# Performance work log

Hardware: AMD Instinct MI355X
Metric: run time of the kernel (lower is better)

Reference implementation:

```python
import jax, jax.numpy as jnp
import numpy as np

NH, DH = 16, 64          # n_head, d_head
CH = NH + DH             # 80
RQ, RK, RV = 6, 2, 2
ROPE_BASE = 10000.0


def _rotary(b, cache_len):
    # b: [B, T, R, DH]; rotates the d-factor exactly as the torch Rotary module
    T = b.shape[1]
    inv_freq = (1.0 / ROPE_BASE) ** (jnp.arange(0, DH, 2, dtype=jnp.float32) / DH)
    t = jnp.arange(T, dtype=jnp.float32) + cache_len
    freqs = jnp.outer(t, inv_freq)                      # [T, DH/2]
    cos = freqs[None, :, None, :].astype(b.dtype)
    sin = jnp.sin(freqs)[None, :, None, :].astype(b.dtype)
    cos = jnp.cos(freqs)[None, :, None, :].astype(b.dtype)
    x1, x2 = jnp.split(b, 2, axis=3)
    return jnp.concatenate([x1 * cos + x2 * sin, -x1 * sin + x2 * cos], axis=3)


def setup_inputs() -> dict:
    key = jax.random.key(0)
    k1, k2, k3, k4 = jax.random.split(key, 4)
    B, T, D = 2, 2048, 1024
    x = jax.random.normal(k1, (B, T, D), dtype=jnp.float32)
    # xavier-uniform-like scale for factor projections
    s_q = float(np.sqrt(6.0 / (D + CH)))
    s_o = float(np.sqrt(6.0 / (D + D)))
    W_abq = jax.random.uniform(k2, (RQ * CH, D), minval=-s_q, maxval=s_q, dtype=jnp.float32)
    W_abkv = jax.random.uniform(k3, ((RK + RV) * CH, D), minval=-s_q, maxval=s_q, dtype=jnp.float32)
    W_o = jax.random.uniform(k4, (D, D), minval=-s_o, maxval=s_o, dtype=jnp.float32)
    return {"x": x, "W_abq": W_abq, "W_abkv": W_abkv, "W_o": W_o}


def reference(x, W_abq, W_abkv, W_o):
    B, T, D = x.shape
    # low-rank factor projections
    abq = (x @ W_abq.T).reshape(B, T, RQ, CH)
    a_q, b_q = abq[..., :NH], abq[..., NH:]            # [B,T,RQ,NH], [B,T,RQ,DH]
    abkv = (x @ W_abkv.T).reshape(B, T, RK + RV, CH)
    a_kv = abkv[..., :NH]
    b_kv = _rotary(abkv[..., NH:], cache_len=0)        # RoPE applied to K/V d-factors only
    a_k, b_k = a_kv[:, :, :RK], b_kv[:, :, :RK]
    a_v, b_v = a_kv[:, :, RK:], b_kv[:, :, RK:]
    # tensor-product reconstruction of Q/K/V
    q = jnp.einsum('btrh,btrd->bthd', a_q, b_q) / RQ
    k = jnp.einsum('btrh,btrd->bthd', a_k, b_k) / RK
    v = jnp.einsum('btrh,btrd->bthd', a_v, b_v) / RV
    # causal attention (flex_attention default scale = 1/sqrt(dh))
    scale = 1.0 / jnp.sqrt(jnp.asarray(DH, dtype=q.dtype))
    scores = jnp.einsum('bqhd,bkhd->bhqk', q, k) * scale
    causal = jnp.tril(jnp.ones((T, T), dtype=bool))
    scores = jnp.where(causal[None, None], scores, jnp.finfo(scores.dtype).min)
    attn = jax.nn.softmax(scores, axis=-1)
    y = jnp.einsum('bhqk,bkhd->bqhd', attn, v).reshape(B, T, D)
    return y @ W_o.T
```

## Files before the change

### kernel.cpp

```cpp
#include <hip/hip_runtime.h>
#include <hip/hip_bf16.h>
#include <math.h>

#define NHEADS 16
#define DHEAD  64
#define CHDIM  80
#define RQn    6
#define RKn    2
#define RVn    2
#define BB     2
#define TT     2048
#define DDim   1024
#define NQK    800

using frag16 = __attribute__((ext_vector_type(8))) short;
using f32x4  = __attribute__((ext_vector_type(4))) float;
using f32x16 = __attribute__((ext_vector_type(16))) float;

#define AS1(p) ((const __attribute__((address_space(1))) unsigned int*)(p))
#define AS3(p) ((__attribute__((address_space(3))) unsigned int*)(p))

static __device__ __forceinline__ unsigned short bf16_bits(float f) {
    __hip_bfloat16 h = __float2bfloat16(f);
    return *(unsigned short*)&h;
}
static __device__ __forceinline__ unsigned int pk2(float a, float b) {
    return ((unsigned int)bf16_bits(b) << 16) | (unsigned int)bf16_bits(a);
}

__global__ __launch_bounds__(256) void cvt_all(
    const float* __restrict__ x, const float* __restrict__ wq,
    const float* __restrict__ wk, const float* __restrict__ wo,
    __hip_bfloat16* __restrict__ xb, __hip_bfloat16* __restrict__ wqk,
    __hip_bfloat16* __restrict__ wob)
{
    int bid = blockIdx.x;
    const float* src; __hip_bfloat16* dst; int n4;
    if (bid < 4096)      { src = x;  dst = xb;            n4 = 1048576; }
    else if (bid < 4576) { bid -= 4096; src = wq; dst = wqk;           n4 = 122880; }
    else if (bid < 4896) { bid -= 4576; src = wk; dst = wqk + 491520;  n4 = 81920; }
    else                 { bid -= 4896; src = wo; dst = wob;           n4 = 262144; }
    int i = bid * 256 + threadIdx.x;
    if (i < n4) {
        float4 v = *(const float4*)&src[i * 4];
        ushort4 o;
        o.x = bf16_bits(v.x); o.y = bf16_bits(v.y);
        o.z = bf16_bits(v.z); o.w = bf16_bits(v.w);
        *(ushort4*)&dst[i * 4] = o;
    }
}

__global__ __launch_bounds__(256) void gemm_bf16(
    const __hip_bfloat16* __restrict__ A, const __hip_bfloat16* __restrict__ W,
    float* __restrict__ C, int M, int N, int K)
{
    __shared__ __hip_bfloat16 Asl[2][128 * 64];
    __shared__ __hip_bfloat16 Bsl[2][128 * 64];
    const int tid = threadIdx.x;
    const int w = tid >> 6, lane = tid & 63;
    const int l16 = lane & 15, quad = lane >> 4;
    const int wr = w >> 1, wc = w & 1;
    const int bm = blockIdx.y * 128, bn = blockIdx.x * 128;

    int rS[4], cS[4], rBS[4];
    #pragma unroll
    for (int j = 0; j < 4; j++) {
        int L = (w * 4 + j) * 64 + lane;
        rS[j] = L >> 3;
        cS[j] = (L & 7) ^ (rS[j] & 7);
        int rb = bn + rS[j];
        rBS[j] = (rb < N) ? rb : (N - 1);
    }

    f32x4 acc[4][4];
    #pragma unroll
    for (int mt = 0; mt < 4; mt++)
        #pragma unroll
        for (int nt = 0; nt < 4; nt++)
            acc[mt][nt] = (f32x4){0.f, 0.f, 0.f, 0.f};

    const int nK = K >> 6;
    #pragma unroll
    for (int j = 0; j < 4; j++) {
        const __hip_bfloat16* ga = A + (size_t)(bm + rS[j]) * K + cS[j] * 8;
        const __hip_bfloat16* gb = W + (size_t)rBS[j] * K + cS[j] * 8;
        __builtin_amdgcn_global_load_lds(AS1(ga), AS3(&Asl[0][(w * 4 + j) * 512]), 16, 0, 0);
        __builtin_amdgcn_global_load_lds(AS1(gb), AS3(&Bsl[0][(w * 4 + j) * 512]), 16, 0, 0);
    }

    for (int kk = 0; kk < nK; kk++) {
        const int cur = kk & 1;
        __syncthreads();
        if (kk + 1 < nK) {
            const int k1 = (kk + 1) * 64;
            #pragma unroll
            for (int j = 0; j < 4; j++) {
                const __hip_bfloat16* ga = A + (size_t)(bm + rS[j]) * K + k1 + cS[j] * 8;
                const __hip_bfloat16* gb = W + (size_t)rBS[j] * K + k1 + cS[j] * 8;
                __builtin_amdgcn_global_load_lds(AS1(ga), AS3(&Asl[cur ^ 1][(w * 4 + j) * 512]), 16, 0, 0);
                __builtin_amdgcn_global_load_lds(AS1(gb), AS3(&Bsl[cur ^ 1][(w * 4 + j) * 512]), 16, 0, 0);
            }
        }
        #pragma unroll
        for (int ks = 0; ks < 2; ks++) {
            frag16 af[4], bf[4];
            #pragma unroll
            for (int mt = 0; mt < 4; mt++) {
                int r = wr * 64 + mt * 16 + l16;
                af[mt] = *(const frag16*)&Asl[cur][r * 64 + (((ks * 4 + quad) ^ (r & 7)) * 8)];
            }
            #pragma unroll
            for (int nt = 0; nt < 4; nt++) {
                int r = wc * 64 + nt * 16 + l16;
                bf[nt] = *(const frag16*)&Bsl[cur][r * 64 + (((ks * 4 + quad) ^ (r & 7)) * 8)];
            }
            #pragma unroll
            for (int mt = 0; mt < 4; mt++)
                #pragma unroll
                for (int nt = 0; nt < 4; nt++)
                    acc[mt][nt] = __builtin_amdgcn_mfma_f32_16x16x32_bf16(af[mt], bf[nt], acc[mt][nt], 0, 0, 0);
        }
    }
    #pragma unroll
    for (int mt = 0; mt < 4; mt++) {
        #pragma unroll
        for (int reg = 0; reg < 4; reg++) {
            int row = bm + wr * 64 + mt * 16 + quad * 4 + reg;
            #pragma unroll
            for (int nt = 0; nt < 4; nt++) {
                int col = bn + wc * 64 + nt * 16 + l16;
                if (col < N) C[(size_t)row * N + col] = acc[mt][nt][reg];
            }
        }
    }
}

__global__ __launch_bounds__(256) void qkv_kernel(
    const float* __restrict__ ab,
    __hip_bfloat16* __restrict__ q, __hip_bfloat16* __restrict__ k,
    __hip_bfloat16* __restrict__ vT)
{
    const int tok0 = blockIdx.x * 4;
    const int w = threadIdx.x >> 6;
    const int d = threadIdx.x & 63;
    const int token = tok0 + w;
    const int b = token / TT;
    const int t = token % TT;
    __shared__ float sq[4][RQn * CHDIM];
    __shared__ float skv[4][(RKn + RVn) * CHDIM];
    __shared__ __align__(8) __hip_bfloat16 vbuf[NHEADS][DHEAD][4];
    const float* aq  = ab + (size_t)token * NQK;
    const float* akv = aq + 480;
    for (int i = d; i < RQn * CHDIM; i += 64) sq[w][i] = aq[i];
    for (int i = d; i < (RKn + RVn) * CHDIM; i += 64) skv[w][i] = akv[i];
    const int i32 = d & 31;
    float inv_freq = powf(10000.0f, -(float)i32 / 32.0f);
    float fr = (float)t * inv_freq;
    float c = cosf(fr), s = sinf(fr);
    float rot[4];
    #pragma unroll
    for (int r = 0; r < 4; r++) {
        float x1 = skv[w][r * CHDIM + NHEADS + i32];
        float x2 = skv[w][r * CHDIM + NHEADS + 32 + i32];
        rot[r] = (d < 32) ? (x1 * c + x2 * s) : (-x1 * s + x2 * c);
    }
    float bqv[RQn];
    #pragma unroll
    for (int r = 0; r < RQn; r++) bqv[r] = sq[w][r * CHDIM + NHEADS + d];
    #pragma unroll
    for (int h = 0; h < NHEADS; h++) {
        float accq = 0.0f;
        #pragma unroll
        for (int r = 0; r < RQn; r++)
            accq += sq[w][r * CHDIM + h] * bqv[r];
        q[((size_t)(b * NHEADS + h) * TT + t) * DHEAD + d] = __float2bfloat16(accq * (0.125f / 6.0f));
        float acck = 0.0f, accv = 0.0f;
        #pragma unroll
        for (int r = 0; r < RKn; r++)
            acck += skv[w][r * CHDIM + h] * rot[r];
        #pragma unroll
        for (int r = 0; r < RVn; r++)
            accv += skv[w][(RKn + r) * CHDIM + h] * rot[RKn + r];
        k[((size_t)(b * NHEADS + h) * TT + t) * DHEAD + d] = __float2bfloat16(acck * 0.5f);
        vbuf[h][d][w] = __float2bfloat16(accv * 0.5f);
    }
    __syncthreads();
    const int t0 = tok0 % TT;
    const int b0 = tok0 / TT;
    for (int row = threadIdx.x; row < NHEADS * DHEAD; row += 256) {
        int h = row >> 6, dd = row & 63;
        *(uint2*)&vT[((size_t)(b0 * NHEADS + h) * DHEAD + dd) * TT + t0] =
            *(const uint2*)&vbuf[h][dd][0];
    }
}

static __device__ __forceinline__ void attn_tile(
    const __hip_bfloat16* __restrict__ Kc, const __hip_bfloat16* __restrict__ Vc,
    const frag16 qB[4], f32x16& O0, f32x16& O1, float& lpart,
    const int l31, const int hi, const int xi, const int paddr,
    const bool domask, const int kb0, const int qlane)
{
    f32x16 ST0 = {}, ST1 = {};
    #pragma unroll
    for (int kt4 = 0; kt4 < 4; kt4++) {
        int c8 = kt4 * 2 + hi;
        frag16 kf0 = *(const frag16*)&Kc[l31 * 64 + ((c8 ^ xi) * 8)];
        frag16 kf1 = *(const frag16*)&Kc[(32 + l31) * 64 + ((c8 ^ xi) * 8)];
        ST0 = __builtin_amdgcn_mfma_f32_32x32x16_bf16(kf0, qB[kt4], ST0, 0, 0, 0);
        ST1 = __builtin_amdgcn_mfma_f32_32x32x16_bf16(kf1, qB[kt4], ST1, 0, 0, 0);
    }
    float* s0 = (float*)&ST0;
    float* s1 = (float*)&ST1;
    if (domask) {
        int kbq = kb0 + 4 * hi;
        #pragma unroll
        for (int reg = 0; reg < 16; reg++) {
            int rowc = (reg & 3) + 8 * (reg >> 2);
            if (kbq + rowc > qlane)      s0[reg] = -1e30f;
            if (kbq + 32 + rowc > qlane) s1[reg] = -1e30f;
        }
    }
    #pragma unroll
    for (int reg = 0; reg < 16; reg++) {
        float p0 = __expf(s0[reg]);
        float p1 = __expf(s1[reg]);
        s0[reg] = p0; s1[reg] = p1;
        lpart += p0 + p1;
    }
    frag16 Pf[4];
    #pragma unroll
    for (int k2 = 0; k2 < 4; k2++) {
        const float* sF = (k2 >= 2) ? s1 : s0;
        const int bs = 8 * (k2 & 1);
        unsigned int u0a = pk2(sF[bs + 0], sF[bs + 1]);
        unsigned int u0b = pk2(sF[bs + 2], sF[bs + 3]);
        unsigned int u1a = pk2(sF[bs + 4], sF[bs + 5]);
        unsigned int u1b = pk2(sF[bs + 6], sF[bs + 7]);
        unsigned int r0a = (unsigned int)__builtin_amdgcn_ds_bpermute(paddr, (int)u0a);
        unsigned int r0b = (unsigned int)__builtin_amdgcn_ds_bpermute(paddr, (int)u0b);
        unsigned int r1a = (unsigned int)__builtin_amdgcn_ds_bpermute(paddr, (int)u1a);
        unsigned int r1b = (unsigned int)__builtin_amdgcn_ds_bpermute(paddr, (int)u1b);
        union { frag16 f; unsigned int u[4]; } pf;
        pf.u[0] = hi ? r1a : u0a;
        pf.u[1] = hi ? r1b : u0b;
        pf.u[2] = hi ? u1a : r0a;
        pf.u[3] = hi ? u1b : r0b;
        Pf[k2] = pf.f;
    }
    #pragma unroll
    for (int k2 = 0; k2 < 4; k2++) {
        int c8 = k2 * 2 + hi;
        frag16 vf0 = *(const frag16*)&Vc[l31 * 64 + ((c8 ^ xi) * 8)];
        frag16 vf1 = *(const frag16*)&Vc[(32 + l31) * 64 + ((c8 ^ xi) * 8)];
        O0 = __builtin_amdgcn_mfma_f32_32x32x16_bf16(vf0, Pf[k2], O0, 0, 0, 0);
        O1 = __builtin_amdgcn_mfma_f32_32x32x16_bf16(vf1, Pf[k2], O1, 0, 0, 0);
    }
}

__global__ __launch_bounds__(256, 2) void flash_mfma(
    const __hip_bfloat16* __restrict__ q, const __hip_bfloat16* __restrict__ k,
    const __hip_bfloat16* __restrict__ vT, __hip_bfloat16* __restrict__ y,
    float* __restrict__ Op, float* __restrict__ Lp)
{
    const int g = blockIdx.x;
    const int bh = g & 31;
    const int pr = g >> 5;
    const int qthalf = pr & 7;
    const int part = pr >> 3;
    const int qt_lo = qthalf, qt_hi = 15 - qthalf;
    const int nlo = 2 * qt_lo + 2;
    const int S = 17 - nlo;
    const int b = bh >> 4, h = bh & 15;
    const int tid = threadIdx.x;
    const int w = tid >> 6;
    const int lane = tid & 63;
    const int l31 = lane & 31;
    const int hi = lane >> 5;
    const int xi = l31 & 7;
    const int paddr = (lane ^ 32) << 2;

    __shared__ __align__(16) __hip_bfloat16 KsF[2][4096];
    __shared__ __align__(16) __hip_bfloat16 VsF[2][4096];

    const size_t base = (size_t)bh * TT * DHEAD;
    const __hip_bfloat16* qb = q + base;
    const __hip_bfloat16* kb = k + base;
    const __hip_bfloat16* vb = vT + base;

    const int ktd_lo = 2 * qt_lo + (w >> 1);
    const int ktd_hi = 2 * qt_hi + (w >> 1);
    const int qlane_lo = qt_lo * 128 + w * 32 + l31;
    const int qlane_hi = qt_hi * 128 + w * 32 + l31;

    const int k0off  = part ? S : 0;
    const int nsteps = part ? 17 : ((nlo > S) ? nlo : S);

    int offK[2], offV[2];
    #pragma unroll
    for (int j = 0; j < 2; j++) {
        int Lc = w * 128 + j * 64 + lane;
        int r = Lc >> 3, c8 = Lc & 7, g8 = c8 ^ (r & 7);
        offK[j] = r * 64 + g8 * 8;
        offV[j] = r * TT + g8 * 8;
    }

    frag16 qB_hi[4], qB_lo[4];
    #pragma unroll
    for (int kt4 = 0; kt4 < 4; kt4++)
        qB_hi[kt4] = *(const frag16*)&qb[(size_t)qlane_hi * DHEAD + kt4 * 16 + hi * 8];
    if (part == 0) {
        #pragma unroll
        for (int kt4 = 0; kt4 < 4; kt4++)
            qB_lo[kt4] = *(const frag16*)&qb[(size_t)qlane_lo * DHEAD + kt4 * 16 + hi * 8];
    }

    f32x16 Olo0 = {}, Olo1 = {}, Ohi0 = {}, Ohi1 = {};
    float l_lo = 0.0f, l_hi = 0.0f;

    #pragma unroll
    for (int j = 0; j < 2; j++) {
        __builtin_amdgcn_global_load_lds(AS1(kb + (size_t)k0off * 4096 + offK[j]),
                                         AS3(&KsF[0][w * 1024 + j * 512]), 16, 0, 0);
        __builtin_amdgcn_global_load_lds(AS1(vb + (size_t)k0off * 64 + offV[j]),
                                         AS3(&VsF[0][w * 1024 + j * 512]), 16, 0, 0);
    }

    for (int kt = 0; kt < nsteps; kt++) {
        const int cur = kt & 1;
        __syncthreads();
        if (kt + 1 < nsteps) {
            const int phys1 = k0off + kt + 1;
            #pragma unroll
            for (int j = 0; j < 2; j++) {
                __builtin_amdgcn_global_load_lds(AS1(kb + (size_t)phys1 * 4096 + offK[j]),
                                                 AS3(&KsF[cur ^ 1][w * 1024 + j * 512]), 16, 0, 0);
                __builtin_amdgcn_global_load_lds(AS1(vb + (size_t)phys1 * 64 + offV[j]),
                                                 AS3(&VsF[cur ^ 1][w * 1024 + j * 512]), 16, 0, 0);
            }
        }
        const __hip_bfloat16* Kc = KsF[cur];
        const __hip_bfloat16* Vc = VsF[cur];
        if (part == 0) {
            if (kt <= ktd_lo)
                attn_tile(Kc, Vc, qB_lo, Olo0, Olo1, l_lo, l31, hi, xi, paddr,
                          kt == ktd_lo, kt * 64, qlane_lo);
            if (kt < S)
                attn_tile(Kc, Vc, qB_hi, Ohi0, Ohi1, l_hi, l31, hi, xi, paddr,
                          false, 0, qlane_hi);
        } else {
            const int phys = S + kt;
            if (phys <= ktd_hi)
                attn_tile(Kc, Vc, qB_hi, Ohi0, Ohi1, l_hi, l31, hi, xi, paddr,
                          phys == ktd_hi, phys * 64, qlane_hi);
        }
    }

    if (part == 0) {
        float lother = __int_as_float(__builtin_amdgcn_ds_bpermute(paddr, __float_as_int(l_lo)));
        float inv = 1.0f / (l_lo + lother);
        float* o0 = (float*)&Olo0;
        float* o1 = (float*)&Olo1;
        __hip_bfloat16* yp = y + ((size_t)(b * TT + qlane_lo)) * DDim + h * DHEAD;
        #pragma unroll
        for (int gg = 0; gg < 4; gg++) {
            int d0 = 8 * gg + 4 * hi;
            uint2 pa, pb;
            pa.x = pk2(o0[4*gg+0] * inv, o0[4*gg+1] * inv);
            pa.y = pk2(o0[4*gg+2] * inv, o0[4*gg+3] * inv);
            pb.x = pk2(o1[4*gg+0] * inv, o1[4*gg+1] * inv);
            pb.y = pk2(o1[4*gg+2] * inv, o1[4*gg+3] * inv);
            *(uint2*)&yp[d0] = pa;
            *(uint2*)&yp[32 + d0] = pb;
        }
    }
    {
        float lother = __int_as_float(__builtin_amdgcn_ds_bpermute(paddr, __float_as_int(l_hi)));
        float ltot = l_hi + lother;
        const int slot = bh * 8 + qthalf;
        const int rloc = w * 32 + l31;
        float* Od = Op + ((size_t)part * 256 + slot) * 8192 + (size_t)rloc * 64;
        float* o0 = (float*)&Ohi0;
        float* o1 = (float*)&Ohi1;
        #pragma unroll
        for (int gg = 0; gg < 4; gg++) {
            int d0 = 8 * gg + 4 * hi;
            *(float4*)&Od[d0]      = (float4){o0[4*gg+0], o0[4*gg+1], o0[4*gg+2], o0[4*gg+3]};
            *(float4*)&Od[32 + d0] = (float4){o1[4*gg+0], o1[4*gg+1], o1[4*gg+2], o1[4*gg+3]};
        }
        if (hi == 0) Lp[part * 32768 + slot * 128 + rloc] = ltot;
    }
}

__global__ __launch_bounds__(256) void combine(
    const float* __restrict__ Op, const float* __restrict__ Lp,
    __hip_bfloat16* __restrict__ y)
{
    int idx = blockIdx.x * 256 + threadIdx.x;
    int slot = idx >> 7, row = idx & 127;
    int bh = slot >> 3, qthalf = slot & 7;
    int b = bh >> 4, h = bh & 15;
    int qrow = (15 - qthalf) * 128 + row;
    float l0 = Lp[slot * 128 + row];
    float l1 = Lp[32768 + slot * 128 + row];
    float inv = 1.0f / (l0 + l1);
    const float* p0 = Op + (size_t)(slot * 128 + row) * 64;
    const float* p1 = p0 + 2097152;
    __hip_bfloat16* yp = y + ((size_t)(b * TT + qrow)) * DDim + h * DHEAD;
    #pragma unroll
    for (int c = 0; c < 64; c += 8) {
        float4 a0 = *(const float4*)&p0[c];
        float4 a1 = *(const float4*)&p0[c + 4];
        float4 b0 = *(const float4*)&p1[c];
        float4 b1 = *(const float4*)&p1[c + 4];
        uint4 o;
        o.x = pk2((a0.x + b0.x) * inv, (a0.y + b0.y) * inv);
        o.y = pk2((a0.z + b0.z) * inv, (a0.w + b0.w) * inv);
        o.z = pk2((a1.x + b1.x) * inv, (a1.y + b1.y) * inv);
        o.w = pk2((a1.z + b1.z) * inv, (a1.w + b1.w) * inv);
        *(uint4*)&yp[c] = o;
    }
}

extern "C" void kernel_launch(void* const* d_in, const int* in_sizes, int n_in,
                              void* d_out, int out_size, void* d_ws, size_t ws_size,
                              hipStream_t stream) {
    const float* x      = (const float*)d_in[0];
    const float* W_abq  = (const float*)d_in[1];
    const float* W_abkv = (const float*)d_in[2];
    const float* W_o    = (const float*)d_in[3];
    float* out = (float*)d_out;

    char* ws = (char*)d_ws;
    __hip_bfloat16* xb   = (__hip_bfloat16*)ws;  ws += (size_t)4194304 * 2;
    __hip_bfloat16* wqk  = (__hip_bfloat16*)ws;  ws += (size_t)NQK * 1024 * 2;
    __hip_bfloat16* wo_b = (__hip_bfloat16*)ws;  ws += (size_t)1048576 * 2;
    float* abqkv = (float*)ws;                   ws += (size_t)4096 * NQK * 4;
    __hip_bfloat16* qb = (__hip_bfloat16*)ws;    ws += (size_t)4194304 * 2;
    __hip_bfloat16* kb = (__hip_bfloat16*)ws;    ws += (size_t)4194304 * 2;
    __hip_bfloat16* vT = (__hip_bfloat16*)ws;    ws += (size_t)4194304 * 2;
    __hip_bfloat16* yb = (__hip_bfloat16*)ws;    ws += (size_t)4194304 * 2;
    float* Op = (float*)ws;                      ws += (size_t)2 * 2097152 * 4;
    float* Lp = (float*)ws;                      ws += (size_t)2 * 32768 * 4;

    cvt_all<<<dim3(5920), dim3(256), 0, stream>>>(x, W_abq, W_abkv, W_o, xb, wqk, wo_b);
    gemm_bf16<<<dim3(7, 32), dim3(256), 0, stream>>>(xb, wqk, abqkv, 4096, NQK, 1024);
    qkv_kernel<<<dim3(1024), dim3(256), 0, stream>>>(abqkv, qb, kb, vT);
    flash_mfma<<<dim3(512), dim3(256), 0, stream>>>(qb, kb, vT, yb, Op, Lp);
    combine<<<dim3(128), dim3(256), 0, stream>>>(Op, Lp, yb);
    gemm_bf16<<<dim3(8, 32), dim3(256), 0, stream>>>(yb, wo_b, out, 4096, 1024, 1024);
}
```

Baseline: 183.8 us.

## Fuse fp32-to-bf16 conversion and split-K combine into GEMM operand loading

```diff
diff --git a/kernel.cpp b/kernel.cpp
--- a/kernel.cpp
+++ b/kernel.cpp
@@ -27,49 +27,37 @@
 static __device__ __forceinline__ unsigned int pk2(float a, float b) {
     return ((unsigned int)bf16_bits(b) << 16) | (unsigned int)bf16_bits(a);
 }
-
-__global__ __launch_bounds__(256) void cvt_all(
-    const float* __restrict__ x, const float* __restrict__ wq,
-    const float* __restrict__ wk, const float* __restrict__ wo,
-    __hip_bfloat16* __restrict__ xb, __hip_bfloat16* __restrict__ wqk,
-    __hip_bfloat16* __restrict__ wob)
+static __device__ __forceinline__ uint4 pk8(const float4& a, const float4& b) {
+    uint4 u;
+    u.x = pk2(a.x, a.y); u.y = pk2(a.z, a.w);
+    u.z = pk2(b.x, b.y); u.w = pk2(b.z, b.w);
+    return u;
+}
+
+__global__ __launch_bounds__(256) void gemm_proj(
+    const float* __restrict__ A, const float* __restrict__ Wq,
+    const float* __restrict__ Wk, float* __restrict__ C)
 {
-    int bid = blockIdx.x;
-    const float* src; __hip_bfloat16* dst; int n4;
-    if (bid < 4096)      { src = x;  dst = xb;            n4 = 1048576; }
-    else if (bid < 4576) { bid -= 4096; src = wq; dst = wqk;           n4 = 122880; }
-    else if (bid < 4896) { bid -= 4576; src = wk; dst = wqk + 491520;  n4 = 81920; }
-    else                 { bid -= 4896; src = wo; dst = wob;           n4 = 262144; }
-    int i = bid * 256 + threadIdx.x;
-    if (i < n4) {
-        float4 v = *(const float4*)&src[i * 4];
-        ushort4 o;
-        o.x = bf16_bits(v.x); o.y = bf16_bits(v.y);
-        o.z = bf16_bits(v.z); o.w = bf16_bits(v.w);
-        *(ushort4*)&dst[i * 4] = o;
-    }
-}
-
-__global__ __launch_bounds__(256) void gemm_bf16(
-    const __hip_bfloat16* __restrict__ A, const __hip_bfloat16* __restrict__ W,
-    float* __restrict__ C, int M, int N, int K)
-{
-    __shared__ __hip_bfloat16 Asl[2][128 * 64];
-    __shared__ __hip_bfloat16 Bsl[2][128 * 64];
+    const int M = 4096, N = NQK, K = 1024;
+    __shared__ __hip_bfloat16 Asl[128 * 64];
+    __shared__ __hip_bfloat16 Bsl[128 * 64];
     const int tid = threadIdx.x;
     const int w = tid >> 6, lane = tid & 63;
     const int l16 = lane & 15, quad = lane >> 4;
     const int wr = w >> 1, wc = w & 1;
     const int bm = blockIdx.y * 128, bn = blockIdx.x * 128;
 
-    int rS[4], cS[4], rBS[4];
+    const float* aP[4]; const float* bP[4]; int ldsOff[4];
     #pragma unroll
     for (int j = 0; j < 4; j++) {
         int L = (w * 4 + j) * 64 + lane;
-        rS[j] = L >> 3;
-        cS[j] = (L & 7) ^ (rS[j] & 7);
-        int rb = bn + rS[j];
-        rBS[j] = (rb < N) ? rb : (N - 1);
+        int r = L >> 3;
+        int c8 = (L & 7) ^ (r & 7);
+        aP[j] = A + (size_t)(bm + r) * K + c8 * 8;
+        int rb = bn + r; if (rb >= N) rb = N - 1;
+        bP[j] = (rb < 480) ? (Wq + (size_t)rb * K + c8 * 8)
+                           : (Wk + (size_t)(rb - 480) * K + c8 * 8);
+        ldsOff[j] = (w * 4 + j) * 512 + lane * 8;
     }
 
     f32x4 acc[4][4];
@@ -79,26 +67,30 @@
         for (int nt = 0; nt < 4; nt++)
             acc[mt][nt] = (f32x4){0.f, 0.f, 0.f, 0.f};
 
+    float4 av[4][2], bv[4][2];
+    #pragma unroll
+    for (int j = 0; j < 4; j++) {
+        av[j][0] = *(const float4*)(aP[j]);     av[j][1] = *(const float4*)(aP[j] + 4);
+        bv[j][0] = *(const float4*)(bP[j]);     bv[j][1] = *(const float4*)(bP[j] + 4);
+    }
+
     const int nK = K >> 6;
-    #pragma unroll
-    for (int j = 0; j < 4; j++) {
-        const __hip_bfloat16* ga = A + (size_t)(bm + rS[j]) * K + cS[j] * 8;
-        const __hip_bfloat16* gb = W + (size_t)rBS[j] * K + cS[j] * 8;
-        __builtin_amdgcn_global_load_lds(AS1(ga), AS3(&Asl[0][(w * 4 + j) * 512]), 16, 0, 0);
-        __builtin_amdgcn_global_load_lds(AS1(gb), AS3(&Bsl[0][(w * 4 + j) * 512]), 16, 0, 0);
-    }
-
     for (int kk = 0; kk < nK; kk++) {
-        const int cur = kk & 1;
+        __syncthreads();
+        #pragma unroll
+        for (int j = 0; j < 4; j++) {
+            *(uint4*)&Asl[ldsOff[j]] = pk8(av[j][0], av[j][1]);
+            *(uint4*)&Bsl[ldsOff[j]] = pk8(bv[j][0], bv[j][1]);
+        }
         __syncthreads();
         if (kk + 1 < nK) {
             const int k1 = (kk + 1) * 64;
             #pragma unroll
             for (int j = 0; j < 4; j++) {
-                const __hip_bfloat16* ga = A + (size_t)(bm + rS[j]) * K + k1 + cS[j] * 8;
-                const __hip_bfloat16* gb = W + (size_t)rBS[j] * K + k1 + cS[j] * 8;
-                __builtin_amdgcn_global_load_lds(AS1(ga), AS3(&Asl[cur ^ 1][(w * 4 + j) * 512]), 16, 0, 0);
-                __builtin_amdgcn_global_load_lds(AS1(gb), AS3(&Bsl[cur ^ 1][(w * 4 + j) * 512]), 16, 0, 0);
+                av[j][0] = *(const float4*)(aP[j] + k1);
+                av[j][1] = *(const float4*)(aP[j] + k1 + 4);
+                bv[j][0] = *(const float4*)(bP[j] + k1);
+                bv[j][1] = *(const float4*)(bP[j] + k1 + 4);
             }
         }
         #pragma unroll
@@ -107,12 +99,12 @@
             #pragma unroll
             for (int mt = 0; mt < 4; mt++) {
                 int r = wr * 64 + mt * 16 + l16;
-                af[mt] = *(const frag16*)&Asl[cur][r * 64 + (((ks * 4 + quad) ^ (r & 7)) * 8)];
+                af[mt] = *(const frag16*)&Asl[r * 64 + (((ks * 4 + quad) ^ (r & 7)) * 8)];
             }
             #pragma unroll
             for (int nt = 0; nt < 4; nt++) {
                 int r = wc * 64 + nt * 16 + l16;
-                bf[nt] = *(const frag16*)&Bsl[cur][r * 64 + (((ks * 4 + quad) ^ (r & 7)) * 8)];
+                bf[nt] = *(const frag16*)&Bsl[r * 64 + (((ks * 4 + quad) ^ (r & 7)) * 8)];
             }
             #pragma unroll
             for (int mt = 0; mt < 4; mt++)
@@ -130,6 +122,153 @@
             for (int nt = 0; nt < 4; nt++) {
                 int col = bn + wc * 64 + nt * 16 + l16;
                 if (col < N) C[(size_t)row * N + col] = acc[mt][nt][reg];
+            }
+        }
+    }
+}
+
+__global__ __launch_bounds__(256) void gemm_out(
+    const __hip_bfloat16* __restrict__ Y, const float* __restrict__ Op,
+    const float* __restrict__ Lp, const float* __restrict__ Wo,
+    float* __restrict__ C)
+{
+    const int N = 1024, K = 1024;
+    __shared__ __hip_bfloat16 Asl[128 * 64];
+    __shared__ __hip_bfloat16 Bsl[128 * 64];
+    const int tid = threadIdx.x;
+    const int w = tid >> 6, lane = tid & 63;
+    const int l16 = lane & 15, quad = lane >> 4;
+    const int wr = w >> 1, wc = w & 1;
+    const int bm = blockIdx.y * 128, bn = blockIdx.x * 128;
+    const int bb = bm >> 11;
+    const int qt = (bm & 2047) >> 7;
+    const bool hiB = (qt >= 8);
+    const int qthalf = 15 - qt;
+
+    int rA[4], c8A[4], ldsOff[4];
+    const float* bP[4];
+    #pragma unroll
+    for (int j = 0; j < 4; j++) {
+        int L = (w * 4 + j) * 64 + lane;
+        int r = L >> 3;
+        int c8 = (L & 7) ^ (r & 7);
+        rA[j] = r; c8A[j] = c8;
+        bP[j] = Wo + (size_t)(bn + r) * K + c8 * 8;
+        ldsOff[j] = (w * 4 + j) * 512 + lane * 8;
+    }
+
+    f32x4 acc[4][4];
+    #pragma unroll
+    for (int mt = 0; mt < 4; mt++)
+        #pragma unroll
+        for (int nt = 0; nt < 4; nt++)
+            acc[mt][nt] = (f32x4){0.f, 0.f, 0.f, 0.f};
+
+    float4 bv[4][2];
+    uint4 uv[4];
+    float4 a0v[4][2], a1v[4][2];
+    float l0v[4], l1v[4];
+
+    #pragma unroll
+    for (int j = 0; j < 4; j++) {
+        bv[j][0] = *(const float4*)(bP[j]);
+        bv[j][1] = *(const float4*)(bP[j] + 4);
+    }
+    if (hiB) {
+        const int slot0 = (bb * 16 + 0) * 8 + qthalf;
+        #pragma unroll
+        for (int j = 0; j < 4; j++) {
+            const float* p0 = Op + (size_t)slot0 * 8192 + rA[j] * 64 + c8A[j] * 8;
+            a0v[j][0] = *(const float4*)(p0);           a0v[j][1] = *(const float4*)(p0 + 4);
+            a1v[j][0] = *(const float4*)(p0 + 2097152); a1v[j][1] = *(const float4*)(p0 + 2097152 + 4);
+            l0v[j] = Lp[slot0 * 128 + rA[j]];
+            l1v[j] = Lp[32768 + slot0 * 128 + rA[j]];
+        }
+    } else {
+        #pragma unroll
+        for (int j = 0; j < 4; j++)
+            uv[j] = *(const uint4*)&Y[(size_t)(bm + rA[j]) * K + c8A[j] * 8];
+    }
+
+    const int nK = K >> 6;
+    for (int kk = 0; kk < nK; kk++) {
+        __syncthreads();
+        #pragma unroll
+        for (int j = 0; j < 4; j++)
+            *(uint4*)&Bsl[ldsOff[j]] = pk8(bv[j][0], bv[j][1]);
+        if (hiB) {
+            #pragma unroll
+            for (int j = 0; j < 4; j++) {
+                float inv = 1.0f / (l0v[j] + l1v[j]);
+                float4 s0, s1;
+                s0.x = (a0v[j][0].x + a1v[j][0].x) * inv;
+                s0.y = (a0v[j][0].y + a1v[j][0].y) * inv;
+                s0.z = (a0v[j][0].z + a1v[j][0].z) * inv;
+                s0.w = (a0v[j][0].w + a1v[j][0].w) * inv;
+                s1.x = (a0v[j][1].x + a1v[j][1].x) * inv;
+                s1.y = (a0v[j][1].y + a1v[j][1].y) * inv;
+                s1.z = (a0v[j][1].z + a1v[j][1].z) * inv;
+                s1.w = (a0v[j][1].w + a1v[j][1].w) * inv;
+                *(uint4*)&Asl[ldsOff[j]] = pk8(s0, s1);
+            }
+        } else {
+            #pragma unroll
+            for (int j = 0; j < 4; j++)
+                *(uint4*)&Asl[ldsOff[j]] = uv[j];
+        }
+        __syncthreads();
+        if (kk + 1 < nK) {
+            const int k1 = (kk + 1) * 64;
+            #pragma unroll
+            for (int j = 0; j < 4; j++) {
+                bv[j][0] = *(const float4*)(bP[j] + k1);
+                bv[j][1] = *(const float4*)(bP[j] + k1 + 4);
+            }
+            if (hiB) {
+                const int slot = (bb * 16 + (kk + 1)) * 8 + qthalf;
+                #pragma unroll
+                for (int j = 0; j < 4; j++) {
+                    const float* p0 = Op + (size_t)slot * 8192 + rA[j] * 64 + c8A[j] * 8;
+                    a0v[j][0] = *(const float4*)(p0);           a0v[j][1] = *(const float4*)(p0 + 4);
+                    a1v[j][0] = *(const float4*)(p0 + 2097152); a1v[j][1] = *(const float4*)(p0 + 2097152 + 4);
+                    l0v[j] = Lp[slot * 128 + rA[j]];
+                    l1v[j] = Lp[32768 + slot * 128 + rA[j]];
+                }
+            } else {
+                #pragma unroll
+                for (int j = 0; j < 4; j++)
+                    uv[j] = *(const uint4*)&Y[(size_t)(bm + rA[j]) * K + k1 + c8A[j] * 8];
+            }
+        }
+        #pragma unroll
+        for (int ks = 0; ks < 2; ks++) {
+            frag16 af[4], bf[4];
+            #pragma unroll
+            for (int mt = 0; mt < 4; mt++) {
+                int r = wr * 64 + mt * 16 + l16;
+                af[mt] = *(const frag16*)&Asl[r * 64 + (((ks * 4 + quad) ^ (r & 7)) * 8)];
+            }
+            #pragma unroll
+            for (int nt = 0; nt < 4; nt++) {
+                int r = wc * 64 + nt * 16 + l16;
+                bf[nt] = *(const frag16*)&Bsl[r * 64 + (((ks * 4 + quad) ^ (r & 7)) * 8)];
+            }
+            #pragma unroll
+            for (int mt = 0; mt < 4; mt++)
+                #pragma unroll
+                for (int nt = 0; nt < 4; nt++)
+                    acc[mt][nt] = __builtin_amdgcn_mfma_f32_16x16x32_bf16(af[mt], bf[nt], acc[mt][nt], 0, 0, 0);
+        }
+    }
+    #pragma unroll
+    for (int mt = 0; mt < 4; mt++) {
+        #pragma unroll
+        for (int reg = 0; reg < 4; reg++) {
+            int row = bm + wr * 64 + mt * 16 + quad * 4 + reg;
+            #pragma unroll
+            for (int nt = 0; nt < 4; nt++) {
+                int col = bn + wc * 64 + nt * 16 + l16;
+                C[(size_t)row * N + col] = acc[mt][nt][reg];
             }
         }
     }
@@ -391,36 +530,6 @@
     }
 }
 
-__global__ __launch_bounds__(256) void combine(
-    const float* __restrict__ Op, const float* __restrict__ Lp,
-    __hip_bfloat16* __restrict__ y)
-{
-    int idx = blockIdx.x * 256 + threadIdx.x;
-    int slot = idx >> 7, row = idx & 127;
-    int bh = slot >> 3, qthalf = slot & 7;
-    int b = bh >> 4, h = bh & 15;
-    int qrow = (15 - qthalf) * 128 + row;
-    float l0 = Lp[slot * 128 + row];
-    float l1 = Lp[32768 + slot * 128 + row];
-    float inv = 1.0f / (l0 + l1);
-    const float* p0 = Op + (size_t)(slot * 128 + row) * 64;
-    const float* p1 = p0 + 2097152;
-    __hip_bfloat16* yp = y + ((size_t)(b * TT + qrow)) * DDim + h * DHEAD;
-    #pragma unroll
-    for (int c = 0; c < 64; c += 8) {
-        float4 a0 = *(const float4*)&p0[c];
-        float4 a1 = *(const float4*)&p0[c + 4];
-        float4 b0 = *(const float4*)&p1[c];
-        float4 b1 = *(const float4*)&p1[c + 4];
-        uint4 o;
-        o.x = pk2((a0.x + b0.x) * inv, (a0.y + b0.y) * inv);
-        o.y = pk2((a0.z + b0.z) * inv, (a0.w + b0.w) * inv);
-        o.z = pk2((a1.x + b1.x) * inv, (a1.y + b1.y) * inv);
-        o.w = pk2((a1.z + b1.z) * inv, (a1.w + b1.w) * inv);
-        *(uint4*)&yp[c] = o;
-    }
-}
-
 extern "C" void kernel_launch(void* const* d_in, const int* in_sizes, int n_in,
                               void* d_out, int out_size, void* d_ws, size_t ws_size,
                               hipStream_t stream) {
@@ -431,9 +540,6 @@
     float* out = (float*)d_out;
 
     char* ws = (char*)d_ws;
-    __hip_bfloat16* xb   = (__hip_bfloat16*)ws;  ws += (size_t)4194304 * 2;
-    __hip_bfloat16* wqk  = (__hip_bfloat16*)ws;  ws += (size_t)NQK * 1024 * 2;
-    __hip_bfloat16* wo_b = (__hip_bfloat16*)ws;  ws += (size_t)1048576 * 2;
     float* abqkv = (float*)ws;                   ws += (size_t)4096 * NQK * 4;
     __hip_bfloat16* qb = (__hip_bfloat16*)ws;    ws += (size_t)4194304 * 2;
     __hip_bfloat16* kb = (__hip_bfloat16*)ws;    ws += (size_t)4194304 * 2;
@@ -442,10 +548,8 @@
     float* Op = (float*)ws;                      ws += (size_t)2 * 2097152 * 4;
     float* Lp = (float*)ws;                      ws += (size_t)2 * 32768 * 4;
 
-    cvt_all<<<dim3(5920), dim3(256), 0, stream>>>(x, W_abq, W_abkv, W_o, xb, wqk, wo_b);
-    gemm_bf16<<<dim3(7, 32), dim3(256), 0, stream>>>(xb, wqk, abqkv, 4096, NQK, 1024);
+    gemm_proj<<<dim3(7, 32), dim3(256), 0, stream>>>(x, W_abq, W_abkv, abqkv);
     qkv_kernel<<<dim3(1024), dim3(256), 0, stream>>>(abqkv, qb, kb, vT);
     flash_mfma<<<dim3(512), dim3(256), 0, stream>>>(qb, kb, vT, yb, Op, Lp);
-    combine<<<dim3(128), dim3(256), 0, stream>>>(Op, Lp, yb);
-    gemm_bf16<<<dim3(8, 32), dim3(256), 0, stream>>>(yb, wo_b, out, 4096, 1024, 1024);
-}
+    gemm_out<<<dim3(8, 32), dim3(256), 0, stream>>>(yb, Op, Lp, W_o, out);
+}
```

Measured after the change: 206.4 us. +12.3%, slower.

## Shrink GEMM M-tile to 64 and share K/V fragments across two query tiles

Applied to the files above, without the earlier changes.

```diff
diff --git a/kernel.cpp b/kernel.cpp
--- a/kernel.cpp
+++ b/kernel.cpp
@@ -54,39 +54,46 @@
     const __hip_bfloat16* __restrict__ A, const __hip_bfloat16* __restrict__ W,
     float* __restrict__ C, int M, int N, int K)
 {
-    __shared__ __hip_bfloat16 Asl[2][128 * 64];
+    __shared__ __hip_bfloat16 Asl[2][64 * 64];
     __shared__ __hip_bfloat16 Bsl[2][128 * 64];
     const int tid = threadIdx.x;
     const int w = tid >> 6, lane = tid & 63;
     const int l16 = lane & 15, quad = lane >> 4;
-    const int wr = w >> 1, wc = w & 1;
-    const int bm = blockIdx.y * 128, bn = blockIdx.x * 128;
-
-    int rS[4], cS[4], rBS[4];
+    const int bm = blockIdx.y * 64, bn = blockIdx.x * 128;
+
+    int rSA[2], cSA[2];
+    #pragma unroll
+    for (int j = 0; j < 2; j++) {
+        int L = (w * 2 + j) * 64 + lane;
+        rSA[j] = L >> 3;
+        cSA[j] = (L & 7) ^ (rSA[j] & 7);
+    }
+    int rSB[4], cSB[4];
     #pragma unroll
     for (int j = 0; j < 4; j++) {
         int L = (w * 4 + j) * 64 + lane;
-        rS[j] = L >> 3;
-        cS[j] = (L & 7) ^ (rS[j] & 7);
-        int rb = bn + rS[j];
-        rBS[j] = (rb < N) ? rb : (N - 1);
-    }
-
-    f32x4 acc[4][4];
+        int r = L >> 3;
+        cSB[j] = (L & 7) ^ (r & 7);
+        int rb = bn + r;
+        rSB[j] = (rb < N) ? rb : (N - 1);
+    }
+
+    f32x4 acc[4][2];
     #pragma unroll
     for (int mt = 0; mt < 4; mt++)
         #pragma unroll
-        for (int nt = 0; nt < 4; nt++)
+        for (int nt = 0; nt < 2; nt++)
             acc[mt][nt] = (f32x4){0.f, 0.f, 0.f, 0.f};
 
     const int nK = K >> 6;
     #pragma unroll
-    for (int j = 0; j < 4; j++) {
-        const __hip_bfloat16* ga = A + (size_t)(bm + rS[j]) * K + cS[j] * 8;
-        const __hip_bfloat16* gb = W + (size_t)rBS[j] * K + cS[j] * 8;
-        __builtin_amdgcn_global_load_lds(AS1(ga), AS3(&Asl[0][(w * 4 + j) * 512]), 16, 0, 0);
-        __builtin_amdgcn_global_load_lds(AS1(gb), AS3(&Bsl[0][(w * 4 + j) * 512]), 16, 0, 0);
-    }
+    for (int j = 0; j < 2; j++)
+        __builtin_amdgcn_global_load_lds(AS1(A + (size_t)(bm + rSA[j]) * K + cSA[j] * 8),
+                                         AS3(&Asl[0][(w * 2 + j) * 512]), 16, 0, 0);
+    #pragma unroll
+    for (int j = 0; j < 4; j++)
+        __builtin_amdgcn_global_load_lds(AS1(W + (size_t)rSB[j] * K + cSB[j] * 8),
+                                         AS3(&Bsl[0][(w * 4 + j) * 512]), 16, 0, 0);
 
     for (int kk = 0; kk < nK; kk++) {
         const int cur = kk & 1;
@@ -94,30 +101,31 @@
         if (kk + 1 < nK) {
             const int k1 = (kk + 1) * 64;
             #pragma unroll
-            for (int j = 0; j < 4; j++) {
-                const __hip_bfloat16* ga = A + (size_t)(bm + rS[j]) * K + k1 + cS[j] * 8;
-                const __hip_bfloat16* gb = W + (size_t)rBS[j] * K + k1 + cS[j] * 8;
-                __builtin_amdgcn_global_load_lds(AS1(ga), AS3(&Asl[cur ^ 1][(w * 4 + j) * 512]), 16, 0, 0);
-                __builtin_amdgcn_global_load_lds(AS1(gb), AS3(&Bsl[cur ^ 1][(w * 4 + j) * 512]), 16, 0, 0);
-            }
+            for (int j = 0; j < 2; j++)
+                __builtin_amdgcn_global_load_lds(AS1(A + (size_t)(bm + rSA[j]) * K + k1 + cSA[j] * 8),
+                                                 AS3(&Asl[cur ^ 1][(w * 2 + j) * 512]), 16, 0, 0);
+            #pragma unroll
+            for (int j = 0; j < 4; j++)
+                __builtin_amdgcn_global_load_lds(AS1(W + (size_t)rSB[j] * K + k1 + cSB[j] * 8),
+                                                 AS3(&Bsl[cur ^ 1][(w * 4 + j) * 512]), 16, 0, 0);
         }
         #pragma unroll
         for (int ks = 0; ks < 2; ks++) {
-            frag16 af[4], bf[4];
+            frag16 af[4], bf[2];
             #pragma unroll
             for (int mt = 0; mt < 4; mt++) {
-                int r = wr * 64 + mt * 16 + l16;
+                int r = mt * 16 + l16;
                 af[mt] = *(const frag16*)&Asl[cur][r * 64 + (((ks * 4 + quad) ^ (r & 7)) * 8)];
             }
             #pragma unroll
-            for (int nt = 0; nt < 4; nt++) {
-                int r = wc * 64 + nt * 16 + l16;
+            for (int nt = 0; nt < 2; nt++) {
+                int r = w * 32 + nt * 16 + l16;
                 bf[nt] = *(const frag16*)&Bsl[cur][r * 64 + (((ks * 4 + quad) ^ (r & 7)) * 8)];
             }
             #pragma unroll
             for (int mt = 0; mt < 4; mt++)
                 #pragma unroll
-                for (int nt = 0; nt < 4; nt++)
+                for (int nt = 0; nt < 2; nt++)
                     acc[mt][nt] = __builtin_amdgcn_mfma_f32_16x16x32_bf16(af[mt], bf[nt], acc[mt][nt], 0, 0, 0);
         }
     }
@@ -125,10 +133,10 @@
     for (int mt = 0; mt < 4; mt++) {
         #pragma unroll
         for (int reg = 0; reg < 4; reg++) {
-            int row = bm + wr * 64 + mt * 16 + quad * 4 + reg;
-            #pragma unroll
-            for (int nt = 0; nt < 4; nt++) {
-                int col = bn + wc * 64 + nt * 16 + l16;
+            int row = bm + mt * 16 + quad * 4 + reg;
+            #pragma unroll
+            for (int nt = 0; nt < 2; nt++) {
+                int col = bn + w * 32 + nt * 16 + l16;
                 if (col < N) C[(size_t)row * N + col] = acc[mt][nt][reg];
             }
         }
@@ -194,40 +202,9 @@
     }
 }
 
-static __device__ __forceinline__ void attn_tile(
-    const __hip_bfloat16* __restrict__ Kc, const __hip_bfloat16* __restrict__ Vc,
-    const frag16 qB[4], f32x16& O0, f32x16& O1, float& lpart,
-    const int l31, const int hi, const int xi, const int paddr,
-    const bool domask, const int kb0, const int qlane)
-{
-    f32x16 ST0 = {}, ST1 = {};
-    #pragma unroll
-    for (int kt4 = 0; kt4 < 4; kt4++) {
-        int c8 = kt4 * 2 + hi;
-        frag16 kf0 = *(const frag16*)&Kc[l31 * 64 + ((c8 ^ xi) * 8)];
-        frag16 kf1 = *(const frag16*)&Kc[(32 + l31) * 64 + ((c8 ^ xi) * 8)];
-        ST0 = __builtin_amdgcn_mfma_f32_32x32x16_bf16(kf0, qB[kt4], ST0, 0, 0, 0);
-        ST1 = __builtin_amdgcn_mfma_f32_32x32x16_bf16(kf1, qB[kt4], ST1, 0, 0, 0);
-    }
-    float* s0 = (float*)&ST0;
-    float* s1 = (float*)&ST1;
-    if (domask) {
-        int kbq = kb0 + 4 * hi;
-        #pragma unroll
-        for (int reg = 0; reg < 16; reg++) {
-            int rowc = (reg & 3) + 8 * (reg >> 2);
-            if (kbq + rowc > qlane)      s0[reg] = -1e30f;
-            if (kbq + 32 + rowc > qlane) s1[reg] = -1e30f;
-        }
-    }
-    #pragma unroll
-    for (int reg = 0; reg < 16; reg++) {
-        float p0 = __expf(s0[reg]);
-        float p1 = __expf(s1[reg]);
-        s0[reg] = p0; s1[reg] = p1;
-        lpart += p0 + p1;
-    }
-    frag16 Pf[4];
+static __device__ __forceinline__ void build_pfrag(
+    const float* s0, const float* s1, frag16 Pf[4], const int hi, const int paddr)
+{
     #pragma unroll
     for (int k2 = 0; k2 < 4; k2++) {
         const float* sF = (k2 >= 2) ? s1 : s0;
@@ -247,6 +224,43 @@
         pf.u[3] = hi ? u1b : r0b;
         Pf[k2] = pf.f;
     }
+}
+
+static __device__ __forceinline__ void attn_tile(
+    const __hip_bfloat16* __restrict__ Kc, const __hip_bfloat16* __restrict__ Vc,
+    const frag16 qB[4], f32x16& O0, f32x16& O1, float& lpart,
+    const int l31, const int hi, const int xi, const int paddr,
+    const bool domask, const int kb0, const int qlane)
+{
+    f32x16 ST0 = {}, ST1 = {};
+    #pragma unroll
+    for (int kt4 = 0; kt4 < 4; kt4++) {
+        int c8 = kt4 * 2 + hi;
+        frag16 kf0 = *(const frag16*)&Kc[l31 * 64 + ((c8 ^ xi) * 8)];
+        frag16 kf1 = *(const frag16*)&Kc[(32 + l31) * 64 + ((c8 ^ xi) * 8)];
+        ST0 = __builtin_amdgcn_mfma_f32_32x32x16_bf16(kf0, qB[kt4], ST0, 0, 0, 0);
+        ST1 = __builtin_amdgcn_mfma_f32_32x32x16_bf16(kf1, qB[kt4], ST1, 0, 0, 0);
+    }
+    float* s0 = (float*)&ST0;
+    float* s1 = (float*)&ST1;
+    if (domask) {
+        int kbq = kb0 + 4 * hi;
+        #pragma unroll
+        for (int reg = 0; reg < 16; reg++) {
+            int rowc = (reg & 3) + 8 * (reg >> 2);
+            if (kbq + rowc > qlane)      s0[reg] = -1e30f;
+            if (kbq + 32 + rowc > qlane) s1[reg] = -1e30f;
+        }
+    }
+    #pragma unroll
+    for (int reg = 0; reg < 16; reg++) {
+        float p0 = __expf(s0[reg]);
+        float p1 = __expf(s1[reg]);
+        s0[reg] = p0; s1[reg] = p1;
+        lpart += p0 + p1;
+    }
+    frag16 Pf[4];
+    build_pfrag(s0, s1, Pf, hi, paddr);
     #pragma unroll
     for (int k2 = 0; k2 < 4; k2++) {
         int c8 = k2 * 2 + hi;
@@ -254,6 +268,58 @@
         frag16 vf1 = *(const frag16*)&Vc[(32 + l31) * 64 + ((c8 ^ xi) * 8)];
         O0 = __builtin_amdgcn_mfma_f32_32x32x16_bf16(vf0, Pf[k2], O0, 0, 0, 0);
         O1 = __builtin_amdgcn_mfma_f32_32x32x16_bf16(vf1, Pf[k2], O1, 0, 0, 0);
+    }
+}
+
+static __device__ __forceinline__ void attn_tile2(
+    const __hip_bfloat16* __restrict__ Kc, const __hip_bfloat16* __restrict__ Vc,
+    const frag16 qBlo[4], const frag16 qBhi[4],
+    f32x16& Olo0, f32x16& Olo1, float& l_lo,
+    f32x16& Ohi0, f32x16& Ohi1, float& l_hi,
+    const int l31, const int hi, const int xi, const int paddr,
+    const bool domask_lo, const int kb0, const int qlane_lo)
+{
+    f32x16 SL0 = {}, SL1 = {}, SH0 = {}, SH1 = {};
+    #pragma unroll
+    for (int kt4 = 0; kt4 < 4; kt4++) {
+        int c8 = kt4 * 2 + hi;
+        frag16 kf0 = *(const frag16*)&Kc[l31 * 64 + ((c8 ^ xi) * 8)];
+        frag16 kf1 = *(const frag16*)&Kc[(32 + l31) * 64 + ((c8 ^ xi) * 8)];
+        SL0 = __builtin_amdgcn_mfma_f32_32x32x16_bf16(kf0, qBlo[kt4], SL0, 0, 0, 0);
+        SH0 = __builtin_amdgcn_mfma_f32_32x32x16_bf16(kf0, qBhi[kt4], SH0, 0, 0, 0);
+        SL1 = __builtin_amdgcn_mfma_f32_32x32x16_bf16(kf1, qBlo[kt4], SL1, 0, 0, 0);
+        SH1 = __builtin_amdgcn_mfma_f32_32x32x16_bf16(kf1, qBhi[kt4], SH1, 0, 0, 0);
+    }
+    float* sl0 = (float*)&SL0; float* sl1 = (float*)&SL1;
+    float* sh0 = (float*)&SH0; float* sh1 = (float*)&SH1;
+    if (domask_lo) {
+        int kbq = kb0 + 4 * hi;
+        #pragma unroll
+        for (int reg = 0; reg < 16; reg++) {
+            int rowc = (reg & 3) + 8 * (reg >> 2);
+            if (kbq + rowc > qlane_lo)      sl0[reg] = -1e30f;
+            if (kbq + 32 + rowc > qlane_lo) sl1[reg] = -1e30f;
+        }
+    }
+    #pragma unroll
+    for (int reg = 0; reg < 16; reg++) {
+        float a = __expf(sl0[reg]); float b = __expf(sl1[reg]);
+        float c = __expf(sh0[reg]); float d = __expf(sh1[reg]);
+        sl0[reg] = a; sl1[reg] = b; sh0[reg] = c; sh1[reg] = d;
+        l_lo += a + b; l_hi += c + d;
+    }
+    frag16 PfL[4], PfH[4];
+    build_pfrag(sl0, sl1, PfL, hi, paddr);
+    build_pfrag(sh0, sh1, PfH, hi, paddr);
+    #pragma unroll
+    for (int k2 = 0; k2 < 4; k2++) {
+        int c8 = k2 * 2 + hi;
+        frag16 vf0 = *(const frag16*)&Vc[l31 * 64 + ((c8 ^ xi) * 8)];
+        frag16 vf1 = *(const frag16*)&Vc[(32 + l31) * 64 + ((c8 ^ xi) * 8)];
+        Olo0 = __builtin_amdgcn_mfma_f32_32x32x16_bf16(vf0, PfL[k2], Olo0, 0, 0, 0);
+        Ohi0 = __builtin_amdgcn_mfma_f32_32x32x16_bf16(vf0, PfH[k2], Ohi0, 0, 0, 0);
+        Olo1 = __builtin_amdgcn_mfma_f32_32x32x16_bf16(vf1, PfL[k2], Olo1, 0, 0, 0);
+        Ohi1 = __builtin_amdgcn_mfma_f32_32x32x16_bf16(vf1, PfH[k2], Ohi1, 0, 0, 0);
     }
 }
 
@@ -341,10 +407,15 @@
         const __hip_bfloat16* Kc = KsF[cur];
         const __hip_bfloat16* Vc = VsF[cur];
         if (part == 0) {
-            if (kt <= ktd_lo)
+            const bool do_lo = (kt <= ktd_lo);
+            const bool do_hi = (kt < S);
+            if (do_lo && do_hi)
+                attn_tile2(Kc, Vc, qB_lo, qB_hi, Olo0, Olo1, l_lo, Ohi0, Ohi1, l_hi,
+                           l31, hi, xi, paddr, kt == ktd_lo, kt * 64, qlane_lo);
+            else if (do_lo)
                 attn_tile(Kc, Vc, qB_lo, Olo0, Olo1, l_lo, l31, hi, xi, paddr,
                           kt == ktd_lo, kt * 64, qlane_lo);
-            if (kt < S)
+            else if (do_hi)
                 attn_tile(Kc, Vc, qB_hi, Ohi0, Ohi1, l_hi, l31, hi, xi, paddr,
                           false, 0, qlane_hi);
         } else {
@@ -443,9 +514,9 @@
     float* Lp = (float*)ws;                      ws += (size_t)2 * 32768 * 4;
 
     cvt_all<<<dim3(5920), dim3(256), 0, stream>>>(x, W_abq, W_abkv, W_o, xb, wqk, wo_b);
-    gemm_bf16<<<dim3(7, 32), dim3(256), 0, stream>>>(xb, wqk, abqkv, 4096, NQK, 1024);
+    gemm_bf16<<<dim3(7, 64), dim3(256), 0, stream>>>(xb, wqk, abqkv, 4096, NQK, 1024);
     qkv_kernel<<<dim3(1024), dim3(256), 0, stream>>>(abqkv, qb, kb, vT);
     flash_mfma<<<dim3(512), dim3(256), 0, stream>>>(qb, kb, vT, yb, Op, Lp);
     combine<<<dim3(128), dim3(256), 0, stream>>>(Op, Lp, yb);
-    gemm_bf16<<<dim3(8, 32), dim3(256), 0, stream>>>(yb, wo_b, out, 4096, 1024, 1024);
-}
+    gemm_bf16<<<dim3(8, 64), dim3(256), 0, stream>>>(yb, wo_b, out, 4096, 1024, 1024);
+}
```

After: 176.7 us. 3.8% less time.
